# Kernel optimization log

Measured on AMD Instinct MI355X. Metric: run time of the kernel, lower is better.

## Reference

```python
import jax, jax.numpy as jnp
import numpy as np


def setup_inputs() -> dict:
    key = jax.random.key(0)
    B, M, L = 65536, 64, 256  # frames, LPC order, analysis window length
    # Build valid autocorrelation sequences (positive-definite Toeplitz)
    # from random signals via FFT: r_k = sum_t x_t x_{t+k}.
    x = jax.random.normal(key, (B, L), dtype=jnp.float32)
    spec = jnp.abs(jnp.fft.rfft(x, n=2 * L, axis=-1)) ** 2
    r = jnp.fft.irfft(spec, n=2 * L, axis=-1)[..., : M + 1] / L
    # small diagonal loading for numerical safety of the solve / sqrt
    r = r.at[..., 0].add(1e-3)
    return {"r": r.astype(jnp.float32)}


def reference(r):
    # r: (..., M+1) autocorrelation. out_format == 'Ka'.
    M = r.shape[-1] - 1
    # Symmetric Toeplitz R[i, j] = r[|i - j|] built by gathering lags.
    idx = jnp.abs(jnp.arange(M)[:, None] - jnp.arange(M)[None, :])  # (M, M)
    R = r[..., :-1][..., idx]  # (..., M, M)
    r1 = r[..., 1:]  # (..., M)
    # a = R^{-1} (-r1); solve is the efficient form of inverse @ vec (same math).
    a = jnp.linalg.solve(R, -r1[..., None])[..., 0]  # (..., M)
    r0 = r[..., 0]
    K = jnp.sqrt(jnp.einsum("...m,...m->...", r1, a) + r0)[..., None]  # (..., 1)
    return jnp.concatenate((K, a), axis=-1)  # (..., M+1)
```

## Files before the change

### kernel.cpp

```cpp
#include <hip/hip_runtime.h>
#include <math.h>


constexpr int M    = 64;
constexpr int EL   = M + 1;
constexpr int LPB  = 4;
constexpr int BT   = 256;
constexpr int ROWS = BT / LPB;

typedef float vf16 __attribute__((ext_vector_type(16)));

#define REP16(X) X(0) X(1) X(2) X(3) X(4) X(5) X(6) X(7) \
                 X(8) X(9) X(10) X(11) X(12) X(13) X(14) X(15)

__global__ __launch_bounds__(BT, 4) void levinson_kernel(const float* __restrict__ rin,
                                                         float* __restrict__ out) {
  __shared__ float smem[ROWS * EL];
  const int tid = threadIdx.x;
  const int b0  = blockIdx.x * ROWS;
  const int nf  = ROWS * EL;
  const size_t base = (size_t)b0 * EL;

  {
    const int n4 = nf >> 2;
    const float4* in4 = reinterpret_cast<const float4*>(rin + base);
    float4* s4 = reinterpret_cast<float4*>(smem);
    for (int i = tid; i < n4; i += BT) s4[i] = in4[i];
  }
  __syncthreads();

  const int row = tid >> 2;
  const int s   = tid & 3;
  const float* rrow = &smem[row * EL];
  const int rbase = 16 * s + 1;

  vf16 rr, aa = {}, bb = {};
#define LDRR(i) rr[i] = rrow[rbase + i];
  REP16(LDRR)
#undef LDRR
  if (s == 0) bb[0] = 1.f;
  float E = rrow[0];

#pragma unroll 2
  for (int m = 1; m <= M; ++m) {
    const float pbb = __shfl_up(bb[15], 1);
    const float paa = __shfl_up(aa[15], 1);

    float p0 = bb[0] * rr[0], p1 = bb[1] * rr[1];
    float p2 = bb[2] * rr[2], p3 = bb[3] * rr[3];
    p0 = fmaf(bb[4],  rr[4],  p0); p1 = fmaf(bb[5],  rr[5],  p1);
    p2 = fmaf(bb[6],  rr[6],  p2); p3 = fmaf(bb[7],  rr[7],  p3);
    p0 = fmaf(bb[8],  rr[8],  p0); p1 = fmaf(bb[9],  rr[9],  p1);
    p2 = fmaf(bb[10], rr[10], p2); p3 = fmaf(bb[11], rr[11], p3);
    p0 = fmaf(bb[12], rr[12], p0); p1 = fmaf(bb[13], rr[13], p1);
    p2 = fmaf(bb[14], rr[14], p2); p3 = fmaf(bb[15], rr[15], p3);
    float acc = (p0 + p1) + (p2 + p3);
    acc += __shfl_xor(acc, 1);
    acc += __shfl_xor(acc, 2);
    const float k = -acc / E;

    vf16 bbs = __builtin_shufflevector(bb, bb, 15, 0, 1, 2, 3, 4, 5, 6, 7,
                                       8, 9, 10, 11, 12, 13, 14);
    vf16 aas = __builtin_shufflevector(aa, aa, 15, 0, 1, 2, 3, 4, 5, 6, 7,
                                       8, 9, 10, 11, 12, 13, 14);
    bbs[0] = pbb;
    aas[0] = paa;

#define UPD(i) { const float na = fmaf(k, bb[i], aa[i]);       \
                 const float nb = fmaf(k, aas[i], bbs[i]);     \
                 aa[i] = na; bb[i] = nb; }
    REP16(UPD)
#undef UPD
    if (s == 0) bb[0] = k;
    E = fmaf(-k * k, E, E);
  }

  __syncthreads();

  {
    float* orow = &smem[row * EL];
    if (s == 0) orow[0] = sqrtf(E);
#define STA(i) orow[rbase + i] = aa[i];
    REP16(STA)
#undef STA
  }
  __syncthreads();

  {
    const int n4 = nf >> 2;
    const float4* s4 = reinterpret_cast<const float4*>(smem);
    float4* out4 = reinterpret_cast<float4*>(out + base);
    for (int i = tid; i < n4; i += BT) out4[i] = s4[i];
  }
}

extern "C" void kernel_launch(void* const* d_in, const int* in_sizes, int n_in,
                              void* d_out, int out_size, void* d_ws, size_t ws_size,
                              hipStream_t stream) {
  const float* r = (const float*)d_in[0];
  float* out = (float*)d_out;
  const int B = in_sizes[0] / EL;
  const int blocks = B / ROWS;
  levinson_kernel<<<blocks, BT, 0, stream>>>(r, out);
}
```

Measured before the change: 107.8 us.

## Split each Levinson row across eight lanes and use fast reciprocal

Each autocorrelation row is now handled by eight threads of eight coefficients each instead of four threads of sixteen. This halves per-thread serial work and registers per recursion step, and raises launch-bounds occupancy from 4 to 8. The cost is one more xor-shuffle reduction per step and twice as many blocks. The division by E is replaced with the hardware approximate reciprocal, and the loop is no longer unrolled. The reciprocal may slightly reduce accuracy.

```diff
diff --git a/kernel.cpp b/kernel.cpp
--- a/kernel.cpp
+++ b/kernel.cpp
@@ -4,74 +4,65 @@
 
 constexpr int M    = 64;
 constexpr int EL   = M + 1;
-constexpr int LPB  = 4;
+constexpr int LPB  = 8;
 constexpr int BT   = 256;
 constexpr int ROWS = BT / LPB;
 
-typedef float vf16 __attribute__((ext_vector_type(16)));
-
-#define REP16(X) X(0) X(1) X(2) X(3) X(4) X(5) X(6) X(7) \
-                 X(8) X(9) X(10) X(11) X(12) X(13) X(14) X(15)
-
-__global__ __launch_bounds__(BT, 4) void levinson_kernel(const float* __restrict__ rin,
+__global__ __launch_bounds__(BT, 8) void levinson_kernel(const float* __restrict__ rin,
                                                          float* __restrict__ out) {
   __shared__ float smem[ROWS * EL];
   const int tid = threadIdx.x;
-  const int b0  = blockIdx.x * ROWS;
-  const int nf  = ROWS * EL;
-  const size_t base = (size_t)b0 * EL;
+  const size_t base = (size_t)blockIdx.x * (ROWS * EL);
 
   {
-    const int n4 = nf >> 2;
+    const int n4 = (ROWS * EL) >> 2;
     const float4* in4 = reinterpret_cast<const float4*>(rin + base);
     float4* s4 = reinterpret_cast<float4*>(smem);
     for (int i = tid; i < n4; i += BT) s4[i] = in4[i];
   }
   __syncthreads();
 
-  const int row = tid >> 2;
-  const int s   = tid & 3;
+  const int row = tid >> 3;
+  const int s   = tid & 7;
   const float* rrow = &smem[row * EL];
-  const int rbase = 16 * s + 1;
+  const int rbase = 8 * s + 1;
 
-  vf16 rr, aa = {}, bb = {};
-#define LDRR(i) rr[i] = rrow[rbase + i];
-  REP16(LDRR)
-#undef LDRR
-  if (s == 0) bb[0] = 1.f;
+  const float rr0 = rrow[rbase + 0], rr1 = rrow[rbase + 1];
+  const float rr2 = rrow[rbase + 2], rr3 = rrow[rbase + 3];
+  const float rr4 = rrow[rbase + 4], rr5 = rrow[rbase + 5];
+  const float rr6 = rrow[rbase + 6], rr7 = rrow[rbase + 7];
+  float aa0 = 0.f, aa1 = 0.f, aa2 = 0.f, aa3 = 0.f;
+  float aa4 = 0.f, aa5 = 0.f, aa6 = 0.f, aa7 = 0.f;
+  float bb0 = (s == 0) ? 1.f : 0.f;
+  float bb1 = 0.f, bb2 = 0.f, bb3 = 0.f;
+  float bb4 = 0.f, bb5 = 0.f, bb6 = 0.f, bb7 = 0.f;
   float E = rrow[0];
 
-#pragma unroll 2
-  for (int m = 1; m <= M; ++m) {
-    const float pbb = __shfl_up(bb[15], 1);
-    const float paa = __shfl_up(aa[15], 1);
+#pragma unroll 1
+  for (int m = 0; m < M; ++m) {
+    const float pbb = __shfl_up(bb7, 1);
+    const float paa = __shfl_up(aa7, 1);
 
-    float p0 = bb[0] * rr[0], p1 = bb[1] * rr[1];
-    float p2 = bb[2] * rr[2], p3 = bb[3] * rr[3];
-    p0 = fmaf(bb[4],  rr[4],  p0); p1 = fmaf(bb[5],  rr[5],  p1);
-    p2 = fmaf(bb[6],  rr[6],  p2); p3 = fmaf(bb[7],  rr[7],  p3);
-    p0 = fmaf(bb[8],  rr[8],  p0); p1 = fmaf(bb[9],  rr[9],  p1);
-    p2 = fmaf(bb[10], rr[10], p2); p3 = fmaf(bb[11], rr[11], p3);
-    p0 = fmaf(bb[12], rr[12], p0); p1 = fmaf(bb[13], rr[13], p1);
-    p2 = fmaf(bb[14], rr[14], p2); p3 = fmaf(bb[15], rr[15], p3);
+    float p0 = bb0 * rr0, p1 = bb1 * rr1, p2 = bb2 * rr2, p3 = bb3 * rr3;
+    p0 = fmaf(bb4, rr4, p0); p1 = fmaf(bb5, rr5, p1);
+    p2 = fmaf(bb6, rr6, p2); p3 = fmaf(bb7, rr7, p3);
     float acc = (p0 + p1) + (p2 + p3);
     acc += __shfl_xor(acc, 1);
     acc += __shfl_xor(acc, 2);
-    const float k = -acc / E;
+    acc += __shfl_xor(acc, 4);
 
-    vf16 bbs = __builtin_shufflevector(bb, bb, 15, 0, 1, 2, 3, 4, 5, 6, 7,
-                                       8, 9, 10, 11, 12, 13, 14);
-    vf16 aas = __builtin_shufflevector(aa, aa, 15, 0, 1, 2, 3, 4, 5, 6, 7,
-                                       8, 9, 10, 11, 12, 13, 14);
-    bbs[0] = pbb;
-    aas[0] = paa;
+    const float k = -acc * __builtin_amdgcn_rcpf(E);
 
-#define UPD(i) { const float na = fmaf(k, bb[i], aa[i]);       \
-                 const float nb = fmaf(k, aas[i], bbs[i]);     \
-                 aa[i] = na; bb[i] = nb; }
-    REP16(UPD)
-#undef UPD
-    if (s == 0) bb[0] = k;
+    aa7 = fmaf(k, bb7, aa7); bb7 = fmaf(k, aa6, bb6);
+    aa6 = fmaf(k, bb6, aa6); bb6 = fmaf(k, aa5, bb5);
+    aa5 = fmaf(k, bb5, aa5); bb5 = fmaf(k, aa4, bb4);
+    aa4 = fmaf(k, bb4, aa4); bb4 = fmaf(k, aa3, bb3);
+    aa3 = fmaf(k, bb3, aa3); bb3 = fmaf(k, aa2, bb2);
+    aa2 = fmaf(k, bb2, aa2); bb2 = fmaf(k, aa1, bb1);
+    aa1 = fmaf(k, bb1, aa1); bb1 = fmaf(k, aa0, bb0);
+    aa0 = fmaf(k, bb0, aa0);
+    bb0 = (s == 0) ? k : fmaf(k, paa, pbb);
+
     E = fmaf(-k * k, E, E);
   }
 
@@ -80,14 +71,15 @@
   {
     float* orow = &smem[row * EL];
     if (s == 0) orow[0] = sqrtf(E);
-#define STA(i) orow[rbase + i] = aa[i];
-    REP16(STA)
-#undef STA
+    orow[rbase + 0] = aa0; orow[rbase + 1] = aa1;
+    orow[rbase + 2] = aa2; orow[rbase + 3] = aa3;
+    orow[rbase + 4] = aa4; orow[rbase + 5] = aa5;
+    orow[rbase + 6] = aa6; orow[rbase + 7] = aa7;
   }
   __syncthreads();
 
   {
-    const int n4 = nf >> 2;
+    const int n4 = (ROWS * EL) >> 2;
     const float4* s4 = reinterpret_cast<const float4*>(smem);
     float4* out4 = reinterpret_cast<float4*>(out + base);
     for (int i = tid; i < n4; i += BT) out4[i] = s4[i];
```

Result: slower. 110.0 us (+2.0%).
